# Kernel tuning notes

Measured on AMD Instinct MI355X. Metric: run time of the kernel, lower is better.

The kernel has to match this reference:

```python
import jax, jax.numpy as jnp
import numpy as np

B, T, C, H = 8, 2048, 1024, 64

def setup_inputs() -> dict:
    key = jax.random.key(0)
    k1, k2, k3, k4 = jax.random.split(key, 4)
    s = 0.02
    return {
        "x": jax.random.normal(k1, (B, T, C), dtype=jnp.float32),
        "Wq": jax.random.normal(k2, (C, H), dtype=jnp.float32) * s,
        "Wk": jax.random.normal(k3, (C, H), dtype=jnp.float32) * s,
        "Wv": jax.random.normal(k4, (C, H), dtype=jnp.float32) * s,
    }

def reference(x, Wq, Wk, Wv):
    # single causal self-attention head (dropout inactive / eval mode)
    q = jnp.einsum('btc,ch->bth', x, Wq)
    k = jnp.einsum('btc,ch->bth', x, Wk)
    v = jnp.einsum('btc,ch->bth', x, Wv)
    scale = k.shape[-1] ** -0.5
    scores = jnp.einsum('bth,bsh->bts', q, k) * scale  # [B,T,T]
    Tn = x.shape[1]
    causal = jnp.tril(jnp.ones((Tn, Tn), dtype=bool))
    scores = jnp.where(causal, scores, jnp.finfo(scores.dtype).min)
    weights = jax.nn.softmax(scores, axis=-1)
    return jnp.einsum('bts,bsh->bth', weights, v)
```

## Files before the change

### kernel.cpp

```cpp
#include <hip/hip_runtime.h>
#include <hip/hip_bf16.h>

#define NB 8
#define NT 2048
#define NC 1024
#define NH 64

typedef __attribute__((ext_vector_type(8))) short bf16x8;
typedef __attribute__((ext_vector_type(4))) short bf16x4;
typedef __attribute__((ext_vector_type(4))) float f32x4;

__device__ __forceinline__ unsigned short f2bf(float f) {
  __hip_bfloat16 h = __float2bfloat16(f);
  return __builtin_bit_cast(unsigned short, h);
}

__device__ __forceinline__ f32x4 mfma32(bf16x8 a, bf16x8 b, f32x4 c) {
  return __builtin_amdgcn_mfma_f32_16x16x32_bf16(a, b, c, 0, 0, 0);
}

#if __has_builtin(__builtin_amdgcn_mfma_f32_16x16x16bf16_1k)
__device__ __forceinline__ f32x4 mfma16(bf16x4 a, bf16x4 b, f32x4 c) {
  return __builtin_amdgcn_mfma_f32_16x16x16bf16_1k(a, b, c, 0, 0, 0);
}
#else
__device__ __forceinline__ f32x4 mfma16(bf16x4 a, bf16x4 b, f32x4 c) {
  asm volatile("v_mfma_f32_16x16x16_bf16 %0, %1, %2, %0\n\ts_nop 7"
               : "+v"(c) : "v"(a), "v"(b));
  return c;
}
#endif

__device__ __forceinline__ void stage16(const void* src, char* lds_base) {
#if __has_builtin(__builtin_amdgcn_global_load_lds)
  __builtin_amdgcn_global_load_lds(
      (const __attribute__((address_space(1))) void*)src,
      (__attribute__((address_space(3))) void*)lds_base, 16, 0, 0);
#endif
}

__global__ __launch_bounds__(256) void wt_kernel(const float* __restrict__ Wq,
                                                 const float* __restrict__ Wk,
                                                 const float* __restrict__ Wv,
                                                 unsigned short* __restrict__ Wt) {
  __shared__ float lds[64][65];
  int wi = blockIdx.x >> 4, kt = blockIdx.x & 15;
  const float* W = (wi == 0) ? Wq : ((wi == 1) ? Wk : Wv);
  float scale = (wi == 0) ? 0.18033688011112043f : 1.0f;
  int tid = threadIdx.x;
#pragma unroll
  for (int i = 0; i < 16; ++i) {
    int idx = tid + i * 256;
    lds[idx >> 6][idx & 63] = W[(size_t)(kt * 64 + (idx >> 6)) * NH + (idx & 63)] * scale;
  }
  __syncthreads();
#pragma unroll
  for (int i = 0; i < 16; ++i) {
    int idx = tid + i * 256;
    int n = idx >> 6, kk = idx & 63;
    Wt[(size_t)(wi * 64 + n) * NC + kt * 64 + kk] = f2bf(lds[kk][n]);
  }
}

__global__ __launch_bounds__(512) void proj_kernel(const float* __restrict__ x,
                                                   const unsigned short* __restrict__ Wt,
                                                   unsigned short* __restrict__ qo,
                                                   unsigned short* __restrict__ ko,
                                                   unsigned short* __restrict__ vo) {
  __shared__ __align__(16) char lds[57344];
  const int woff[2] = {0, 24576};
  const int xoff[2] = {49152, 53248};

  int tid = threadIdx.x;
  int lane = tid & 63, w = tid >> 6;
  int ln = lane & 15, g = lane >> 4;
  int rf = w & 1;
  int cs = w >> 1;
  int row0 = blockIdx.x * 32;
  int nc = cs * 16 + ln;

  int srow = tid >> 4, si = tid & 15;
  const float* xsrc = x + (size_t)(row0 + srow) * NC + si * 4;
  int xwb = (srow * 128 + (((si >> 1) ^ (srow & 7)) << 4) + (si & 1) * 8);

  int wl_row = lane >> 3;
  int wl_sg = (lane & 7) ^ wl_row;

  f32x4 acc[3];
#pragma unroll
  for (int j = 0; j < 3; ++j) acc[j] = (f32x4){0.f, 0.f, 0.f, 0.f};

  float4 R0 = *(const float4*)(xsrc);
#pragma unroll
  for (int t = 0; t < 3; ++t) {
    int tt = w + t * 8;
    int mat = tt >> 3, ii = tt & 7;
    stage16(Wt + (size_t)(mat * 64 + ii * 8 + wl_row) * NC + wl_sg * 8,
            lds + woff[0] + mat * 8192 + ii * 1024);
  }
  {
    bf16x4 b4;
    b4[0] = (short)f2bf(R0.x); b4[1] = (short)f2bf(R0.y);
    b4[2] = (short)f2bf(R0.z); b4[3] = (short)f2bf(R0.w);
    *(bf16x4*)(lds + xoff[0] + xwb) = b4;
  }
  R0 = *(const float4*)(xsrc + 64);
  __syncthreads();

#pragma unroll 1
  for (int p = 0; p < 16; ++p) {
    if (p < 15) {
#pragma unroll
      for (int t = 0; t < 3; ++t) {
        int tt = w + t * 8;
        int mat = tt >> 3, ii = tt & 7;
        stage16(Wt + (size_t)(mat * 64 + ii * 8 + wl_row) * NC + (p + 1) * 64 + wl_sg * 8,
                lds + woff[(p + 1) & 1] + mat * 8192 + ii * 1024);
      }
      bf16x4 b4;
      b4[0] = (short)f2bf(R0.x); b4[1] = (short)f2bf(R0.y);
      b4[2] = (short)f2bf(R0.z); b4[3] = (short)f2bf(R0.w);
      *(bf16x4*)(lds + xoff[(p + 1) & 1] + xwb) = b4;
    }
    if (p < 14) {
      R0 = *(const float4*)(xsrc + (p + 2) * 64);
    }
    const char* xc = lds + xoff[p & 1];
    const char* wc = lds + woff[p & 1];
#pragma unroll
    for (int c0 = 0; c0 < 64; c0 += 32) {
      int row = rf * 16 + ln;
      int axb = row * 128 + ((c0 * 2 + g * 16) ^ ((ln & 7) << 4));
      bf16x8 a = *(const bf16x8*)(xc + axb);
      int kg = (c0 >> 3) + g;
      int wb = nc * 128 + ((kg ^ (ln & 7)) << 4);
      bf16x8 bq = *(const bf16x8*)(wc + wb);
      bf16x8 bk = *(const bf16x8*)(wc + 8192 + wb);
      bf16x8 bv = *(const bf16x8*)(wc + 16384 + wb);
      acc[0] = mfma32(a, bq, acc[0]);
      acc[1] = mfma32(a, bk, acc[1]);
      acc[2] = mfma32(a, bv, acc[2]);
    }
    __syncthreads();
  }

  unsigned short(*vlds)[40] = (unsigned short(*)[40])lds;
#pragma unroll
  for (int r = 0; r < 4; ++r) {
    int row = row0 + rf * 16 + g * 4 + r;
    qo[(size_t)row * NH + nc] = f2bf(acc[0][r]);
    ko[(size_t)row * NH + nc] = f2bf(acc[1][r]);
    vlds[nc][rf * 16 + g * 4 + r] = f2bf(acc[2][r]);
  }
  __syncthreads();
  if (tid < 256) {
    int b = row0 / NT, t0b = row0 % NT;
    int hh = tid >> 2, ts = (tid & 3) * 8;
    *(bf16x8*)(vo + (size_t)(b * NH + hh) * NT + t0b + ts) = *(const bf16x8*)&vlds[hh][ts];
  }
}

__global__ __launch_bounds__(256) void attn_kernel(const unsigned short* __restrict__ qw,
                                                   const unsigned short* __restrict__ kw,
                                                   const unsigned short* __restrict__ vw,
                                                   float* __restrict__ out) {
  __shared__ float mbuf[3][64][36];
  __shared__ float olds[32][68];

  int tid = threadIdx.x;
  int lane = tid & 63, ks = tid >> 6;
  int ln = lane & 15, g = lane >> 4;
  int bid = blockIdx.x;
  int b = bid & 7;
  int s = bid >> 3;
  int qtile = (s < 32) ? s : 95 - s;
  int t0 = qtile * 32;
  int tqA = t0 + ln, tqB = t0 + 16 + ln;

  const unsigned short* qpA = qw + (size_t)(b * NT + tqA) * NH + g * 8;
  const unsigned short* qpB = qw + (size_t)(b * NT + tqB) * NH + g * 8;
  bf16x8 qa0 = *(const bf16x8*)(qpA);
  bf16x8 qa1 = *(const bf16x8*)(qpA + 32);
  bf16x8 qb0 = *(const bf16x8*)(qpB);
  bf16x8 qb1 = *(const bf16x8*)(qpB + 32);

  const unsigned short* kb = kw + (size_t)b * NT * NH + g * 8;
  const unsigned short* vb = vw + (size_t)b * NH * NT;

  f32x4 oaccA[4], oaccB[4];
#pragma unroll
  for (int i = 0; i < 4; ++i) {
    oaccA[i] = (f32x4){0.f, 0.f, 0.f, 0.f};
    oaccB[i] = (f32x4){0.f, 0.f, 0.f, 0.f};
  }
  float lA = 0.f, lB = 0.f;

  bf16x8 kc0[4], kc1[4];
#pragma unroll
  for (int st = 0; st < 4; ++st) {
    const unsigned short* kp = kb + (size_t)(ks * 64 + st * 16 + ln) * NH;
    kc0[st] = *(const bf16x8*)(kp);
    kc1[st] = *(const bf16x8*)(kp + 32);
  }

  int send = t0 + 32;
#pragma unroll 1
  for (int s0 = ks * 64; s0 < send; s0 += 256) {
    bf16x4 va[4][4];
#pragma unroll
    for (int hf = 0; hf < 4; ++hf) {
      const unsigned short* vp = vb + (size_t)(hf * 16 + ln) * NT + s0 + g * 4;
#pragma unroll
      for (int st = 0; st < 4; ++st) va[hf][st] = *(const bf16x4*)(vp + st * 16);
    }
    f32x4 sA[4], sB[4];
#pragma unroll
    for (int st = 0; st < 4; ++st) {
      f32x4 a = (f32x4){0.f, 0.f, 0.f, 0.f};
      a = mfma32(kc0[st], qa0, a);
      a = mfma32(kc1[st], qa1, a);
      sA[st] = a;
      f32x4 c = (f32x4){0.f, 0.f, 0.f, 0.f};
      c = mfma32(kc0[st], qb0, c);
      c = mfma32(kc1[st], qb1, c);
      sB[st] = c;
    }
    if (s0 + 256 < send) {
#pragma unroll
      for (int st = 0; st < 4; ++st) {
        const unsigned short* kp = kb + (size_t)(s0 + 256 + st * 16 + ln) * NH;
        kc0[st] = *(const bf16x8*)(kp);
        kc1[st] = *(const bf16x8*)(kp + 32);
      }
    }
    if (s0 + 63 > t0) {
#pragma unroll
      for (int st = 0; st < 4; ++st)
#pragma unroll
        for (int r = 0; r < 4; ++r)
          if (s0 + st * 16 + g * 4 + r > tqA) sA[st][r] = -1e30f;
    }
    if (s0 + 63 > t0 + 16) {
#pragma unroll
      for (int st = 0; st < 4; ++st)
#pragma unroll
        for (int r = 0; r < 4; ++r)
          if (s0 + st * 16 + g * 4 + r > tqB) sB[st][r] = -1e30f;
    }
    bf16x4 pA[4], pB[4];
#pragma unroll
    for (int st = 0; st < 4; ++st)
#pragma unroll
      for (int r = 0; r < 4; ++r) {
        float p = exp2f(sA[st][r]);
        lA += p;
        pA[st][r] = (short)f2bf(p);
        float q2 = exp2f(sB[st][r]);
        lB += q2;
        pB[st][r] = (short)f2bf(q2);
      }

#pragma unroll
    for (int hf = 0; hf < 4; ++hf)
#pragma unroll
      for (int st = 0; st < 4; ++st) {
        oaccA[hf] = mfma16(va[hf][st], pA[st], oaccA[hf]);
        oaccB[hf] = mfma16(va[hf][st], pB[st], oaccB[hf]);
      }
  }

  lA += __shfl_xor(lA, 16);
  lA += __shfl_xor(lA, 32);
  lB += __shfl_xor(lB, 16);
  lB += __shfl_xor(lB, 32);

  if (ks) {
    float* d = mbuf[ks - 1][lane];
    d[0] = lA; d[1] = lB;
#pragma unroll
    for (int hf = 0; hf < 4; ++hf)
#pragma unroll
      for (int r = 0; r < 4; ++r) {
        d[2 + hf * 4 + r] = oaccA[hf][r];
        d[18 + hf * 4 + r] = oaccB[hf][r];
      }
  }
  __syncthreads();
  if (ks == 0) {
#pragma unroll
    for (int j = 0; j < 3; ++j) {
      const float* d = mbuf[j][lane];
      lA += d[0];
      lB += d[1];
#pragma unroll
      for (int hf = 0; hf < 4; ++hf)
#pragma unroll
        for (int r = 0; r < 4; ++r) {
          oaccA[hf][r] += d[2 + hf * 4 + r];
          oaccB[hf][r] += d[18 + hf * 4 + r];
        }
    }
    float invA = 1.f / lA, invB = 1.f / lB;
#pragma unroll
    for (int hf = 0; hf < 4; ++hf)
#pragma unroll
      for (int r = 0; r < 4; ++r) {
        olds[ln][hf * 16 + g * 4 + r] = oaccA[hf][r] * invA;
        olds[16 + ln][hf * 16 + g * 4 + r] = oaccB[hf][r] * invB;
      }
  }
  __syncthreads();
  if (tid < 128) {
    int tl = tid >> 2, h0 = (tid & 3) * 16;
    size_t obase = (size_t)(b * NT + t0 + tl) * NH + h0;
#pragma unroll
    for (int vv = 0; vv < 4; ++vv) {
      float4 t4 = make_float4(olds[tl][h0 + vv * 4 + 0], olds[tl][h0 + vv * 4 + 1],
                              olds[tl][h0 + vv * 4 + 2], olds[tl][h0 + vv * 4 + 3]);
      *(float4*)(out + obase + vv * 4) = t4;
    }
  }
}

extern "C" void kernel_launch(void* const* d_in, const int* in_sizes, int n_in,
                              void* d_out, int out_size, void* d_ws, size_t ws_size,
                              hipStream_t stream) {
  const float* x  = (const float*)d_in[0];
  const float* Wq = (const float*)d_in[1];
  const float* Wk = (const float*)d_in[2];
  const float* Wv = (const float*)d_in[3];
  float* out = (float*)d_out;

  unsigned short* Wt = (unsigned short*)d_ws;
  unsigned short* q  = (unsigned short*)((char*)d_ws + (1 << 19));
  unsigned short* k  = q + (size_t)NB * NT * NH;
  unsigned short* v  = k + (size_t)NB * NT * NH;

  wt_kernel<<<48, 256, 0, stream>>>(Wq, Wk, Wv, Wt);
  proj_kernel<<<(NB * NT) / 32, 512, 0, stream>>>(x, Wt, q, k, v);
  attn_kernel<<<512, 256, 0, stream>>>(q, k, v, out);
}
```

Before: 51.61 us.

## Store K and V in MFMA-fragment-ordered layout for coalesced attention loads

```diff
diff --git a/kernel.cpp b/kernel.cpp
--- a/kernel.cpp
+++ b/kernel.cpp
@@ -38,6 +38,7 @@
       (__attribute__((address_space(3))) void*)lds_base, 16, 0, 0);
 #endif
 }
+
 
 __global__ __launch_bounds__(256) void wt_kernel(const float* __restrict__ Wq,
                                                  const float* __restrict__ Wk,
@@ -65,8 +66,8 @@
 __global__ __launch_bounds__(512) void proj_kernel(const float* __restrict__ x,
                                                    const unsigned short* __restrict__ Wt,
                                                    unsigned short* __restrict__ qo,
-                                                   unsigned short* __restrict__ ko,
-                                                   unsigned short* __restrict__ vo) {
+                                                   unsigned short* __restrict__ kf,
+                                                   unsigned short* __restrict__ vf) {
   __shared__ __align__(16) char lds[57344];
   const int woff[2] = {0, 24576};
   const int xoff[2] = {49152, 53248};
@@ -145,24 +146,33 @@
   }
 
   unsigned short(*vlds)[40] = (unsigned short(*)[40])lds;
+  int bb = row0 >> 11;
 #pragma unroll
   for (int r = 0; r < 4; ++r) {
     int row = row0 + rf * 16 + g * 4 + r;
+    int rib = row & 2047;
     qo[(size_t)row * NH + nc] = f2bf(acc[0][r]);
-    ko[(size_t)row * NH + nc] = f2bf(acc[1][r]);
+    int koff = ((rib >> 4) << 10) + ((nc >> 5) << 9) + (((nc >> 3) & 3) << 7) +
+               ((rib & 15) << 3) + (nc & 7);
+    kf[(size_t)bb * 131072 + koff] = f2bf(acc[1][r]);
     vlds[nc][rf * 16 + g * 4 + r] = f2bf(acc[2][r]);
   }
   __syncthreads();
   if (tid < 256) {
-    int b = row0 / NT, t0b = row0 % NT;
+    int t0b = row0 & 2047;
     int hh = tid >> 2, ts = (tid & 3) * 8;
-    *(bf16x8*)(vo + (size_t)(b * NH + hh) * NT + t0b + ts) = *(const bf16x8*)&vlds[hh][ts];
+    const unsigned short* src = &vlds[hh][ts];
+    int t1 = t0b + ts;
+    size_t vbase = (size_t)bb * 131072 + ((size_t)(t1 >> 4) << 10) + ((hh >> 4) << 8);
+    int g0 = (t1 & 15) >> 2;
+    *(bf16x4*)(vf + vbase + ((g0 * 16 + (hh & 15)) << 2)) = *(const bf16x4*)src;
+    *(bf16x4*)(vf + vbase + (((g0 + 1) * 16 + (hh & 15)) << 2)) = *(const bf16x4*)(src + 4);
   }
 }
 
 __global__ __launch_bounds__(256) void attn_kernel(const unsigned short* __restrict__ qw,
-                                                   const unsigned short* __restrict__ kw,
-                                                   const unsigned short* __restrict__ vw,
+                                                   const unsigned short* __restrict__ kf,
+                                                   const unsigned short* __restrict__ vf,
                                                    float* __restrict__ out) {
   __shared__ float mbuf[3][64][36];
   __shared__ float olds[32][68];
@@ -184,8 +194,8 @@
   bf16x8 qb0 = *(const bf16x8*)(qpB);
   bf16x8 qb1 = *(const bf16x8*)(qpB + 32);
 
-  const unsigned short* kb = kw + (size_t)b * NT * NH + g * 8;
-  const unsigned short* vb = vw + (size_t)b * NH * NT;
+  const unsigned short* kfb = kf + (size_t)b * 131072;
+  const unsigned short* vfb = vf + (size_t)b * 131072;
 
   f32x4 oaccA[4], oaccB[4];
 #pragma unroll
@@ -198,9 +208,9 @@
   bf16x8 kc0[4], kc1[4];
 #pragma unroll
   for (int st = 0; st < 4; ++st) {
-    const unsigned short* kp = kb + (size_t)(ks * 64 + st * 16 + ln) * NH;
+    const unsigned short* kp = kfb + (size_t)((ks * 4) + st) * 1024 + lane * 8;
     kc0[st] = *(const bf16x8*)(kp);
-    kc1[st] = *(const bf16x8*)(kp + 32);
+    kc1[st] = *(const bf16x8*)(kp + 512);
   }
 
   int send = t0 + 32;
@@ -208,10 +218,10 @@
   for (int s0 = ks * 64; s0 < send; s0 += 256) {
     bf16x4 va[4][4];
 #pragma unroll
-    for (int hf = 0; hf < 4; ++hf) {
-      const unsigned short* vp = vb + (size_t)(hf * 16 + ln) * NT + s0 + g * 4;
-#pragma unroll
-      for (int st = 0; st < 4; ++st) va[hf][st] = *(const bf16x4*)(vp + st * 16);
+    for (int st = 0; st < 4; ++st) {
+      const unsigned short* vp = vfb + (size_t)((s0 >> 4) + st) * 1024 + lane * 4;
+#pragma unroll
+      for (int hf = 0; hf < 4; ++hf) va[hf][st] = *(const bf16x4*)(vp + hf * 256);
     }
     f32x4 sA[4], sB[4];
 #pragma unroll
@@ -228,9 +238,9 @@
     if (s0 + 256 < send) {
 #pragma unroll
       for (int st = 0; st < 4; ++st) {
-        const unsigned short* kp = kb + (size_t)(s0 + 256 + st * 16 + ln) * NH;
+        const unsigned short* kp = kfb + (size_t)(((s0 + 256) >> 4) + st) * 1024 + lane * 8;
         kc0[st] = *(const bf16x8*)(kp);
-        kc1[st] = *(const bf16x8*)(kp + 32);
+        kc1[st] = *(const bf16x8*)(kp + 512);
       }
     }
     if (s0 + 63 > t0) {
```

After: 42.62 us, median of 2. 1.21x faster.
